# Kernel optimization log

Measured on AMD Instinct MI355X. Metric: run time of the kernel, lower is better.

Reference implementation:

```python
import jax, jax.numpy as jnp
import numpy as np

SOS = 1  # parsed_vocab.index('<SOS>')
D = 1024
V_IN = 8000
V_OUT = 8000


def gru_cell(x, h, W_ih, W_hh, b_ih, b_hh):
    # PyTorch GRU cell: gates ordered [r, z, n]
    gi = x @ W_ih.T + b_ih          # [B, 3D]
    gh = h @ W_hh.T + b_hh          # [B, 3D]
    i_r, i_z, i_n = jnp.split(gi, 3, axis=-1)
    h_r, h_z, h_n = jnp.split(gh, 3, axis=-1)
    r = jax.nn.sigmoid(i_r + h_r)
    z = jax.nn.sigmoid(i_z + h_z)
    n = jnp.tanh(i_n + r * h_n)
    return (1.0 - z) * n + z * h


def setup_inputs() -> dict:
    key = jax.random.key(0)
    ks = jax.random.split(key, 16)
    s = 1.0 / np.sqrt(D)
    f = lambda k, shape: jax.random.uniform(k, shape, jnp.float32, -s, s)
    return {
        "src": jax.random.randint(ks[0], (256, 128), 0, V_IN),
        "tgt": jax.random.randint(ks[1], (128, 128), 0, V_OUT),
        "enc_emb": jax.random.normal(ks[2], (V_IN, D), jnp.float32),
        "enc_W_ih": f(ks[3], (3 * D, D)),
        "enc_W_hh": f(ks[4], (3 * D, D)),
        "enc_b_ih": f(ks[5], (3 * D,)),
        "enc_b_hh": f(ks[6], (3 * D,)),
        "dec_emb": jax.random.normal(ks[7], (V_OUT, D), jnp.float32),
        "dec_W_ih": f(ks[8], (3 * D, D)),
        "dec_W_hh": f(ks[9], (3 * D, D)),
        "dec_b_ih": f(ks[10], (3 * D,)),
        "dec_b_hh": f(ks[11], (3 * D,)),
        "out_W": f(ks[12], (V_OUT, D)),
        "out_b": f(ks[13], (V_OUT,)),
    }


def reference(src, tgt, enc_emb, enc_W_ih, enc_W_hh, enc_b_ih, enc_b_hh,
              dec_emb, dec_W_ih, dec_W_hh, dec_b_ih, dec_b_hh, out_W, out_b):
    B = src.shape[1]
    # ---- Encoder: GRU over src, keep final hidden ----
    xs = enc_emb[src]  # [S_src, B, D]
    h0 = jnp.zeros((B, D), xs.dtype)

    def enc_step(h, x):
        return gru_cell(x, h, enc_W_ih, enc_W_hh, enc_b_ih, enc_b_hh), None

    h_enc, _ = jax.lax.scan(enc_step, h0, xs)

    # ---- Decoder: greedy argmax feedback (eval path, tf_ratio=0) ----
    tok0 = jnp.full((B,), SOS, dtype=src.dtype)

    def dec_step(carry, _):
        h, tok = carry
        x = dec_emb[tok]                                  # [B, D]
        h_new = gru_cell(x, h, dec_W_ih, dec_W_hh, dec_b_ih, dec_b_hh)
        logits = h_new @ out_W.T + out_b                  # [B, V_OUT]
        next_tok = jnp.argmax(logits, axis=-1).astype(tok.dtype)
        return (h_new, next_tok), logits

    target_length = tgt.shape[0]
    _, logits = jax.lax.scan(dec_step, (h_enc, tok0), None, length=target_length)
    return logits  # [S_tgt, B, V_OUT]
```

## Files before the change

### kernel.cpp

```cpp
#include <hip/hip_runtime.h>
#include <math.h>

#define DD    1024
#define BB    128
#define G3    3072
#define VOUT  8000
#define S_SRC 256
#define S_TGT 128
#define SOS   1
#define KS    4
#define KSL   2

__global__ __launch_bounds__(256) void k_init(float* __restrict__ h, int* __restrict__ tok) {
    int idx = blockIdx.x * 256 + threadIdx.x;
    if (idx < BB * DD) h[idx] = 0.0f;
    if (idx < BB) tok[idx] = SOS;
}

__device__ __forceinline__ void gemm_core(
    const float* __restrict__ A0, const float* __restrict__ A1,
    const float* __restrict__ A2, const float* __restrict__ A3,
    const float* __restrict__ Brow, int kbeg, int ntiles,
    float (&acc)[8][2])
{
    __shared__ float As[32][132];
    __shared__ float Bs[32][36];
    const int tid = threadIdx.x;
    const int kq  = (tid & 7) * 4;
    const int r0  = tid >> 3;
    const int tx  = tid & 15, ty = tid >> 4;
    const float* Arow[4] = {A0, A1, A2, A3};

    for (int t = 0; t < ntiles; ++t) {
        const int k0 = kbeg + t * 32;
        #pragma unroll
        for (int p = 0; p < 4; ++p) {
            float4 v = *reinterpret_cast<const float4*>(Arow[p] + k0 + kq);
            int m = r0 + p * 32;
            As[kq+0][m] = v.x; As[kq+1][m] = v.y; As[kq+2][m] = v.z; As[kq+3][m] = v.w;
        }
        {
            float4 v = *reinterpret_cast<const float4*>(Brow + k0 + kq);
            Bs[kq+0][r0] = v.x; Bs[kq+1][r0] = v.y; Bs[kq+2][r0] = v.z; Bs[kq+3][r0] = v.w;
        }
        __syncthreads();
        #pragma unroll
        for (int k = 0; k < 32; ++k) {
            float a[8];
            #pragma unroll
            for (int i = 0; i < 8; ++i) a[i] = As[k][ty*8 + i];
            float b0 = Bs[k][tx*2 + 0], b1 = Bs[k][tx*2 + 1];
            #pragma unroll
            for (int i = 0; i < 8; ++i) {
                acc[i][0] = fmaf(a[i], b0, acc[i][0]);
                acc[i][1] = fmaf(a[i], b1, acc[i][1]);
            }
        }
        __syncthreads();
    }
}

__global__ __launch_bounds__(256) void k_gi_chunk(
    const float* __restrict__ emb, const int* __restrict__ src_c,
    const float* __restrict__ Wih, const float* __restrict__ bih,
    float* __restrict__ gi_buf)
{
    const int n0    = blockIdx.x * 32;
    const int mbase = blockIdx.y * 128;
    const int tid = threadIdx.x;
    const int r0  = tid >> 3;
    const int tx  = tid & 15, ty = tid >> 4;

    const float* A[4];
    #pragma unroll
    for (int p = 0; p < 4; ++p)
        A[p] = emb + (size_t)src_c[mbase + r0 + p * 32] * DD;
    const float* Brow = Wih + (size_t)(n0 + r0) * DD;

    float acc[8][2] = {};
    gemm_core(A[0], A[1], A[2], A[3], Brow, 0, DD / 32, acc);

    #pragma unroll
    for (int i = 0; i < 8; ++i) {
        size_t m = (size_t)(mbase + ty*8 + i);
        #pragma unroll
        for (int j = 0; j < 2; ++j) {
            int n = n0 + tx*2 + j;
            gi_buf[m * G3 + n] = acc[i][j] + bih[n];
        }
    }
}

__global__ __launch_bounds__(256) void k_gates_ks(
    const float* __restrict__ emb, const int* __restrict__ tok,
    const float* __restrict__ h,
    const float* __restrict__ Wih, const float* __restrict__ Whh,
    float* __restrict__ gi_base, float* __restrict__ gh_base,
    int side_base)
{
    const int side = side_base + blockIdx.y;
    const int kh   = blockIdx.z;
    const int kseg = DD / KS;
    const float* __restrict__ W = side ? Whh : Wih;
    float* __restrict__ C = (side ? gh_base : gi_base) + (size_t)kh * (BB * G3);

    const int n0  = blockIdx.x * 32;
    const int tid = threadIdx.x;
    const int r0  = tid >> 3;
    const int tx  = tid & 15, ty = tid >> 4;

    const float* A[4];
    #pragma unroll
    for (int p = 0; p < 4; ++p) {
        int m = r0 + p * 32;
        A[p] = side ? (h + (size_t)m * DD)
                    : (emb + (size_t)tok[m] * DD);
    }
    const float* Brow = W + (size_t)(n0 + r0) * DD;

    float acc[8][2] = {};
    gemm_core(A[0], A[1], A[2], A[3], Brow, kh * kseg, kseg / 32, acc);

    #pragma unroll
    for (int i = 0; i < 8; ++i) {
        size_t m = (size_t)(ty*8 + i);
        C[m * G3 + n0 + tx*2 + 0] = acc[i][0];
        C[m * G3 + n0 + tx*2 + 1] = acc[i][1];
    }
}

__global__ __launch_bounds__(256) void k_logits_ks(
    const float* __restrict__ h, const float* __restrict__ W,
    float* __restrict__ p_base)
{
    const int kh   = blockIdx.y;
    const int kseg = DD / KSL;
    float* __restrict__ C = p_base + (size_t)kh * (BB * VOUT);

    const int n0  = blockIdx.x * 32;
    const int tid = threadIdx.x;
    const int r0  = tid >> 3;
    const int tx  = tid & 15, ty = tid >> 4;

    const float* A[4];
    #pragma unroll
    for (int p = 0; p < 4; ++p) A[p] = h + (size_t)(r0 + p * 32) * DD;
    const float* Brow = W + (size_t)(n0 + r0) * DD;

    float acc[8][2] = {};
    gemm_core(A[0], A[1], A[2], A[3], Brow, kh * kseg, kseg / 32, acc);

    #pragma unroll
    for (int i = 0; i < 8; ++i) {
        size_t m = (size_t)(ty*8 + i);
        C[m * VOUT + n0 + tx*2 + 0] = acc[i][0];
        C[m * VOUT + n0 + tx*2 + 1] = acc[i][1];
    }
}

__global__ __launch_bounds__(256) void k_update(
    const float* __restrict__ gi_base, int ns_i, const float* __restrict__ bih,
    const float* __restrict__ gh_base, int ns_h, const float* __restrict__ bhh,
    float* __restrict__ h)
{
    int idx = blockIdx.x * 256 + threadIdx.x;
    int b = idx >> 10, d = idx & 1023;
    size_t o = (size_t)b * G3 + d;

    float ir = 0.f, iz = 0.f, in_ = 0.f;
    for (int p = 0; p < ns_i; ++p) {
        const float* g = gi_base + (size_t)p * (BB * G3);
        ir += g[o]; iz += g[o + DD]; in_ += g[o + 2*DD];
    }
    if (bih) { ir += bih[d]; iz += bih[DD + d]; in_ += bih[2*DD + d]; }

    float hr = 0.f, hz = 0.f, hn = 0.f;
    for (int p = 0; p < ns_h; ++p) {
        const float* g = gh_base + (size_t)p * (BB * G3);
        hr += g[o]; hz += g[o + DD]; hn += g[o + 2*DD];
    }
    hr += bhh[d]; hz += bhh[DD + d]; hn += bhh[2*DD + d];

    float r = 1.0f / (1.0f + expf(-(ir + hr)));
    float z = 1.0f / (1.0f + expf(-(iz + hz)));
    float n = tanhf(in_ + r * hn);
    float hv = h[idx];
    h[idx] = (1.0f - z) * n + z * hv;
}

__global__ __launch_bounds__(256) void k_argmax_out(
    const float* __restrict__ p0, const float* __restrict__ p1,
    const float* __restrict__ bias,
    float* __restrict__ outC, int* __restrict__ tok)
{
    const int b = blockIdx.x;
    const size_t ro = (size_t)b * VOUT;
    const int tid = threadIdx.x;

    float bv = -INFINITY; int bi = 0x7fffffff;
    for (int v = tid * 4; v < VOUT; v += 1024) {
        float4 a = *reinterpret_cast<const float4*>(p0 + ro + v);
        float4 c = *reinterpret_cast<const float4*>(p1 + ro + v);
        float4 bb = *reinterpret_cast<const float4*>(bias + v);
        float4 r;
        r.x = a.x + c.x + bb.x;
        r.y = a.y + c.y + bb.y;
        r.z = a.z + c.z + bb.z;
        r.w = a.w + c.w + bb.w;
        *reinterpret_cast<float4*>(outC + ro + v) = r;
        if (r.x > bv) { bv = r.x; bi = v + 0; }
        if (r.y > bv) { bv = r.y; bi = v + 1; }
        if (r.z > bv) { bv = r.z; bi = v + 2; }
        if (r.w > bv) { bv = r.w; bi = v + 3; }
    }
    __shared__ float sv[256];
    __shared__ int   si[256];
    sv[tid] = bv; si[tid] = bi;
    __syncthreads();
    for (int s = 128; s > 0; s >>= 1) {
        if (tid < s) {
            if (sv[tid+s] > sv[tid] || (sv[tid+s] == sv[tid] && si[tid+s] < si[tid])) {
                sv[tid] = sv[tid+s]; si[tid] = si[tid+s];
            }
        }
        __syncthreads();
    }
    if (tid == 0) tok[b] = si[0];
}

extern "C" void kernel_launch(void* const* d_in, const int* in_sizes, int n_in,
                              void* d_out, int out_size, void* d_ws, size_t ws_size,
                              hipStream_t stream) {
    const int*   src     = (const int*)  d_in[0];
    const float* enc_emb = (const float*)d_in[2];
    const float* eWih    = (const float*)d_in[3];
    const float* eWhh    = (const float*)d_in[4];
    const float* ebih    = (const float*)d_in[5];
    const float* ebhh    = (const float*)d_in[6];
    const float* dec_emb = (const float*)d_in[7];
    const float* dWih    = (const float*)d_in[8];
    const float* dWhh    = (const float*)d_in[9];
    const float* dbih    = (const float*)d_in[10];
    const float* dbhh    = (const float*)d_in[11];
    const float* outW    = (const float*)d_in[12];
    const float* outb    = (const float*)d_in[13];
    float* out = (float*)d_out;

    float* h    = (float*)d_ws;
    float* gi_p = h + BB * DD;
    float* gh_p = gi_p + KS * BB * G3;
    int*  tok   = (int*)(gh_p + KS * BB * G3);
    float* scratch = (float*)(tok + 256);

    size_t fixed_bytes = (size_t)((char*)scratch - (char*)d_ws);
    int CH = 8;
    while (CH > 1) {
        size_t scr = (size_t)CH * BB * G3;
        size_t scr2 = (size_t)KSL * BB * VOUT;
        if (scr < scr2) scr = scr2;
        if (fixed_bytes + scr * sizeof(float) <= ws_size) break;
        CH >>= 1;
    }
    float* gi_buf = scratch;
    float* p0     = scratch;
    float* p1     = scratch + BB * VOUT;

    k_init<<<512, 256, 0, stream>>>(h, tok);

    for (int c = 0; c < S_SRC; c += CH) {
        k_gi_chunk<<<dim3(96, CH), 256, 0, stream>>>(enc_emb, src + c * BB,
                                                     eWih, ebih, gi_buf);
        for (int s = 0; s < CH; ++s) {
            k_gates_ks<<<dim3(96, 1, KS), 256, 0, stream>>>(enc_emb, tok, h,
                                                            eWih, eWhh,
                                                            nullptr, gh_p, 1);
            k_update<<<512, 256, 0, stream>>>(gi_buf + (size_t)s * BB * G3, 1, nullptr,
                                              gh_p, KS, ebhh, h);
        }
    }

    for (int t = 0; t < S_TGT; ++t) {
        k_gates_ks<<<dim3(96, 2, KS), 256, 0, stream>>>(dec_emb, tok, h,
                                                        dWih, dWhh,
                                                        gi_p, gh_p, 0);
        k_update<<<512, 256, 0, stream>>>(gi_p, KS, dbih, gh_p, KS, dbhh, h);
        k_logits_ks<<<dim3(250, KSL), 256, 0, stream>>>(h, outW, p0);
        float* Ct = out + (size_t)t * BB * VOUT;
        k_argmax_out<<<128, 256, 0, stream>>>(p0, p1, outb, Ct, tok);
    }
}
```

Baseline: 21.16 ms.

## Replace per-step kernel launches with persistent encoder/decoder kernels using grid barriers

```diff
diff --git a/kernel.cpp b/kernel.cpp
--- a/kernel.cpp
+++ b/kernel.cpp
@@ -8,23 +8,37 @@
 #define S_SRC 256
 #define S_TGT 128
 #define SOS   1
-#define KS    4
-#define KSL   2
-
-__global__ __launch_bounds__(256) void k_init(float* __restrict__ h, int* __restrict__ tok) {
+#define GRID  768
+#define KS_F  4
+
+__device__ __forceinline__ void gbar(unsigned* bar) {
+    __syncthreads();
+    if (threadIdx.x == 0) {
+        __threadfence();
+        unsigned old = atomicAdd(bar, 1u);
+        unsigned target = (old / GRID + 1u) * GRID;
+        while (__hip_atomic_load(bar, __ATOMIC_RELAXED, __HIP_MEMORY_SCOPE_AGENT) < target)
+            __builtin_amdgcn_s_sleep(1);
+        __threadfence();
+    }
+    __syncthreads();
+}
+
+__global__ __launch_bounds__(256) void k_init(float* __restrict__ h, int* __restrict__ tok,
+                                              unsigned* __restrict__ bar) {
     int idx = blockIdx.x * 256 + threadIdx.x;
     if (idx < BB * DD) h[idx] = 0.0f;
     if (idx < BB) tok[idx] = SOS;
+    if (idx == 0) bar[0] = 0u;
 }
 
 __device__ __forceinline__ void gemm_core(
+    float (* __restrict__ As)[132], float (* __restrict__ Bs)[34],
     const float* __restrict__ A0, const float* __restrict__ A1,
     const float* __restrict__ A2, const float* __restrict__ A3,
     const float* __restrict__ Brow, int kbeg, int ntiles,
     float (&acc)[8][2])
 {
-    __shared__ float As[32][132];
-    __shared__ float Bs[32][36];
     const int tid = threadIdx.x;
     const int kq  = (tid & 7) * 4;
     const int r0  = tid >> 3;
@@ -60,26 +74,231 @@
     }
 }
 
+
+__global__ __launch_bounds__(256, 3) void k_enc_p(
+    const float* __restrict__ emb, const int* __restrict__ src,
+    const float* __restrict__ Wih, const float* __restrict__ bih,
+    const float* __restrict__ Whh, const float* __restrict__ bhh,
+    float* __restrict__ h, float* __restrict__ gh_p,
+    float* __restrict__ gi_buf, int CH, unsigned* bar)
+{
+    __shared__ float As[32][132];
+    __shared__ float Bs[32][34];
+    const int bid = blockIdx.x, tid = threadIdx.x;
+    const int r0 = tid >> 3, tx = tid & 15, ty = tid >> 4;
+
+    for (int s = 0; s < S_SRC; ++s) {
+        if ((s & (CH - 1)) == 0) {
+            const int cs = bid / 96, nt = bid % 96;
+            if (cs < CH) {
+                const int* srow = src + (s + cs) * BB;
+                const float* A0 = emb + (size_t)srow[r0 +  0] * DD;
+                const float* A1 = emb + (size_t)srow[r0 + 32] * DD;
+                const float* A2 = emb + (size_t)srow[r0 + 64] * DD;
+                const float* A3 = emb + (size_t)srow[r0 + 96] * DD;
+                float acc[8][2] = {};
+                gemm_core(As, Bs, A0, A1, A2, A3,
+                          Wih + (size_t)(nt*32 + r0) * DD, 0, DD/32, acc);
+                float* C = gi_buf + (size_t)cs * (BB * G3);
+                #pragma unroll
+                for (int i = 0; i < 8; ++i) {
+                    int m = ty*8 + i;
+                    #pragma unroll
+                    for (int j = 0; j < 2; ++j) {
+                        int n = nt*32 + tx*2 + j;
+                        C[(size_t)m * G3 + n] = acc[i][j] + bih[n];
+                    }
+                }
+            }
+            gbar(bar);
+        }
+        {
+            const int kh = bid / 96, nt = bid % 96;
+            const float* A0 = h + (size_t)(r0 +  0) * DD;
+            const float* A1 = h + (size_t)(r0 + 32) * DD;
+            const float* A2 = h + (size_t)(r0 + 64) * DD;
+            const float* A3 = h + (size_t)(r0 + 96) * DD;
+            float acc[8][2] = {};
+            gemm_core(As, Bs, A0, A1, A2, A3,
+                      Whh + (size_t)(nt*32 + r0) * DD, kh * 128, 4, acc);
+            float* C = gh_p + (size_t)kh * (BB * G3);
+            #pragma unroll
+            for (int i = 0; i < 8; ++i) {
+                int m = ty*8 + i;
+                C[(size_t)m * G3 + nt*32 + tx*2 + 0] = acc[i][0];
+                C[(size_t)m * G3 + nt*32 + tx*2 + 1] = acc[i][1];
+            }
+        }
+        gbar(bar);
+        {
+            int idx = bid * 256 + tid;
+            if (idx < BB * DD) {
+                int b = idx >> 10, d = idx & 1023;
+                size_t o = (size_t)b * G3 + d;
+                const float* gib = gi_buf + (size_t)(s & (CH-1)) * (BB * G3);
+                float ir = gib[o], iz = gib[o + DD], in_ = gib[o + 2*DD];
+                float hr = bhh[d], hz = bhh[DD + d], hn = bhh[2*DD + d];
+                #pragma unroll
+                for (int p = 0; p < 8; ++p) {
+                    const float* g = gh_p + (size_t)p * (BB * G3);
+                    hr += g[o]; hz += g[o + DD]; hn += g[o + 2*DD];
+                }
+                float r = 1.0f / (1.0f + expf(-(ir + hr)));
+                float z = 1.0f / (1.0f + expf(-(iz + hz)));
+                float n = tanhf(in_ + r * hn);
+                h[idx] = (1.0f - z) * n + z * h[idx];
+            }
+        }
+        gbar(bar);
+    }
+}
+
+__global__ __launch_bounds__(256, 3) void k_dec_p(
+    const float* __restrict__ emb,
+    const float* __restrict__ Wih, const float* __restrict__ bih,
+    const float* __restrict__ Whh, const float* __restrict__ bhh,
+    const float* __restrict__ outW, const float* __restrict__ outb,
+    float* __restrict__ h, float* __restrict__ g_p,
+    float* __restrict__ lg_p, int* __restrict__ tok,
+    float* __restrict__ out, int KSL, unsigned* bar)
+{
+    __shared__ float As[32][132];
+    __shared__ float Bs[32][34];
+    float* sv = &As[0][0];
+    int*   si = (int*)&As[8][0];
+    const int bid = blockIdx.x, tid = threadIdx.x;
+    const int r0 = tid >> 3, tx = tid & 15, ty = tid >> 4;
+
+    for (int t = 0; t < S_TGT; ++t) {
+        {
+            const int side = bid / 384;
+            const int rem  = bid - side * 384;
+            const int kh   = rem / 96, nt = rem % 96;
+            const float *A0, *A1, *A2, *A3;
+            if (side) {
+                A0 = h + (size_t)(r0 +  0) * DD;
+                A1 = h + (size_t)(r0 + 32) * DD;
+                A2 = h + (size_t)(r0 + 64) * DD;
+                A3 = h + (size_t)(r0 + 96) * DD;
+            } else {
+                A0 = emb + (size_t)tok[r0 +  0] * DD;
+                A1 = emb + (size_t)tok[r0 + 32] * DD;
+                A2 = emb + (size_t)tok[r0 + 64] * DD;
+                A3 = emb + (size_t)tok[r0 + 96] * DD;
+            }
+            const float* W = side ? Whh : Wih;
+            float acc[8][2] = {};
+            gemm_core(As, Bs, A0, A1, A2, A3,
+                      W + (size_t)(nt*32 + r0) * DD, kh * 256, 8, acc);
+            float* C = g_p + (size_t)(side*4 + kh) * (BB * G3);
+            #pragma unroll
+            for (int i = 0; i < 8; ++i) {
+                int m = ty*8 + i;
+                C[(size_t)m * G3 + nt*32 + tx*2 + 0] = acc[i][0];
+                C[(size_t)m * G3 + nt*32 + tx*2 + 1] = acc[i][1];
+            }
+        }
+        gbar(bar);
+        {
+            int idx = bid * 256 + tid;
+            if (idx < BB * DD) {
+                int b = idx >> 10, d = idx & 1023;
+                size_t o = (size_t)b * G3 + d;
+                float ir = bih[d], iz = bih[DD + d], in_ = bih[2*DD + d];
+                #pragma unroll
+                for (int p = 0; p < 4; ++p) {
+                    const float* g = g_p + (size_t)p * (BB * G3);
+                    ir += g[o]; iz += g[o + DD]; in_ += g[o + 2*DD];
+                }
+                float hr = bhh[d], hz = bhh[DD + d], hn = bhh[2*DD + d];
+                #pragma unroll
+                for (int p = 4; p < 8; ++p) {
+                    const float* g = g_p + (size_t)p * (BB * G3);
+                    hr += g[o]; hz += g[o + DD]; hn += g[o + 2*DD];
+                }
+                float r = 1.0f / (1.0f + expf(-(ir + hr)));
+                float z = 1.0f / (1.0f + expf(-(iz + hz)));
+                float n = tanhf(in_ + r * hn);
+                h[idx] = (1.0f - z) * n + z * h[idx];
+            }
+        }
+        gbar(bar);
+        {
+            const int kh = bid / 250, nt = bid % 250;
+            if (kh < KSL) {
+                const int t0 = (32 * kh) / KSL, t1 = (32 * (kh + 1)) / KSL;
+                const float* A0 = h + (size_t)(r0 +  0) * DD;
+                const float* A1 = h + (size_t)(r0 + 32) * DD;
+                const float* A2 = h + (size_t)(r0 + 64) * DD;
+                const float* A3 = h + (size_t)(r0 + 96) * DD;
+                float acc[8][2] = {};
+                gemm_core(As, Bs, A0, A1, A2, A3,
+                          outW + (size_t)(nt*32 + r0) * DD, t0 * 32, t1 - t0, acc);
+                float* C = lg_p + (size_t)kh * (BB * VOUT);
+                #pragma unroll
+                for (int i = 0; i < 8; ++i) {
+                    int m = ty*8 + i;
+                    C[(size_t)m * VOUT + nt*32 + tx*2 + 0] = acc[i][0];
+                    C[(size_t)m * VOUT + nt*32 + tx*2 + 1] = acc[i][1];
+                }
+            }
+        }
+        gbar(bar);
+        if (bid < BB) {
+            const int b = bid;
+            const size_t ro = (size_t)b * VOUT;
+            float* Ct = out + (size_t)t * (BB * VOUT) + ro;
+            float bv = -INFINITY; int bi = 0x7fffffff;
+            for (int v = tid * 4; v < VOUT; v += 1024) {
+                float4 rr = *reinterpret_cast<const float4*>(outb + v);
+                for (int kh = 0; kh < KSL; ++kh) {
+                    float4 p = *reinterpret_cast<const float4*>(
+                        lg_p + (size_t)kh * (BB * VOUT) + ro + v);
+                    rr.x += p.x; rr.y += p.y; rr.z += p.z; rr.w += p.w;
+                }
+                *reinterpret_cast<float4*>(Ct + v) = rr;
+                if (rr.x > bv) { bv = rr.x; bi = v + 0; }
+                if (rr.y > bv) { bv = rr.y; bi = v + 1; }
+                if (rr.z > bv) { bv = rr.z; bi = v + 2; }
+                if (rr.w > bv) { bv = rr.w; bi = v + 3; }
+            }
+            sv[tid] = bv; si[tid] = bi;
+            __syncthreads();
+            for (int st = 128; st > 0; st >>= 1) {
+                if (tid < st) {
+                    if (sv[tid+st] > sv[tid] ||
+                        (sv[tid+st] == sv[tid] && si[tid+st] < si[tid])) {
+                        sv[tid] = sv[tid+st]; si[tid] = si[tid+st];
+                    }
+                }
+                __syncthreads();
+            }
+            if (tid == 0) tok[b] = si[0];
+        }
+        gbar(bar);
+    }
+}
+
+
 __global__ __launch_bounds__(256) void k_gi_chunk(
     const float* __restrict__ emb, const int* __restrict__ src_c,
     const float* __restrict__ Wih, const float* __restrict__ bih,
     float* __restrict__ gi_buf)
 {
+    __shared__ float As[32][132];
+    __shared__ float Bs[32][34];
     const int n0    = blockIdx.x * 32;
     const int mbase = blockIdx.y * 128;
     const int tid = threadIdx.x;
-    const int r0  = tid >> 3;
-    const int tx  = tid & 15, ty = tid >> 4;
+    const int r0  = tid >> 3, tx = tid & 15, ty = tid >> 4;
 
     const float* A[4];
     #pragma unroll
     for (int p = 0; p < 4; ++p)
         A[p] = emb + (size_t)src_c[mbase + r0 + p * 32] * DD;
-    const float* Brow = Wih + (size_t)(n0 + r0) * DD;
-
     float acc[8][2] = {};
-    gemm_core(A[0], A[1], A[2], A[3], Brow, 0, DD / 32, acc);
-
+    gemm_core(As, Bs, A[0], A[1], A[2], A[3],
+              Wih + (size_t)(n0 + r0) * DD, 0, DD/32, acc);
     #pragma unroll
     for (int i = 0; i < 8; ++i) {
         size_t m = (size_t)(mbase + ty*8 + i);
@@ -98,29 +317,27 @@
     float* __restrict__ gi_base, float* __restrict__ gh_base,
     int side_base)
 {
+    __shared__ float As[32][132];
+    __shared__ float Bs[32][34];
     const int side = side_base + blockIdx.y;
     const int kh   = blockIdx.z;
-    const int kseg = DD / KS;
+    const int kseg = DD / KS_F;
     const float* __restrict__ W = side ? Whh : Wih;
     float* __restrict__ C = (side ? gh_base : gi_base) + (size_t)kh * (BB * G3);
 
     const int n0  = blockIdx.x * 32;
     const int tid = threadIdx.x;
-    const int r0  = tid >> 3;
-    const int tx  = tid & 15, ty = tid >> 4;
+    const int r0  = tid >> 3, tx = tid & 15, ty = tid >> 4;
 
     const float* A[4];
     #pragma unroll
     for (int p = 0; p < 4; ++p) {
         int m = r0 + p * 32;
-        A[p] = side ? (h + (size_t)m * DD)
-                    : (emb + (size_t)tok[m] * DD);
-    }
-    const float* Brow = W + (size_t)(n0 + r0) * DD;
-
+        A[p] = side ? (h + (size_t)m * DD) : (emb + (size_t)tok[m] * DD);
+    }
     float acc[8][2] = {};
-    gemm_core(A[0], A[1], A[2], A[3], Brow, kh * kseg, kseg / 32, acc);
-
+    gemm_core(As, Bs, A[0], A[1], A[2], A[3],
+              W + (size_t)(n0 + r0) * DD, kh * kseg, kseg / 32, acc);
     #pragma unroll
     for (int i = 0; i < 8; ++i) {
         size_t m = (size_t)(ty*8 + i);
@@ -133,23 +350,22 @@
     const float* __restrict__ h, const float* __restrict__ W,
     float* __restrict__ p_base)
 {
+    __shared__ float As[32][132];
+    __shared__ float Bs[32][34];
     const int kh   = blockIdx.y;
-    const int kseg = DD / KSL;
+    const int kseg = DD / 2;
     float* __restrict__ C = p_base + (size_t)kh * (BB * VOUT);
 
     const int n0  = blockIdx.x * 32;
     const int tid = threadIdx.x;
-    const int r0  = tid >> 3;
-    const int tx  = tid & 15, ty = tid >> 4;
+    const int r0  = tid >> 3, tx = tid & 15, ty = tid >> 4;
 
     const float* A[4];
     #pragma unroll
     for (int p = 0; p < 4; ++p) A[p] = h + (size_t)(r0 + p * 32) * DD;
-    const float* Brow = W + (size_t)(n0 + r0) * DD;
-
     float acc[8][2] = {};
-    gemm_core(A[0], A[1], A[2], A[3], Brow, kh * kseg, kseg / 32, acc);
-
+    gemm_core(As, Bs, A[0], A[1], A[2], A[3],
+              W + (size_t)(n0 + r0) * DD, kh * kseg, kseg / 32, acc);
     #pragma unroll
     for (int i = 0; i < 8; ++i) {
         size_t m = (size_t)(ty*8 + i);
@@ -158,7 +374,7 @@
     }
 }
 
-__global__ __launch_bounds__(256) void k_update(
+__global__ __launch_bounds__(256) void k_update_f(
     const float* __restrict__ gi_base, int ns_i, const float* __restrict__ bih,
     const float* __restrict__ gh_base, int ns_h, const float* __restrict__ bhh,
     float* __restrict__ h)
@@ -247,45 +463,66 @@
     float* out = (float*)d_out;
 
     float* h    = (float*)d_ws;
-    float* gi_p = h + BB * DD;
-    float* gh_p = gi_p + KS * BB * G3;
-    int*  tok   = (int*)(gh_p + KS * BB * G3);
+    float* g_p  = h + BB * DD;
+    int*  tok   = (int*)(g_p + 8 * BB * G3);
+    unsigned* bar = (unsigned*)(tok + 128);
     float* scratch = (float*)(tok + 256);
 
-    size_t fixed_bytes = (size_t)((char*)scratch - (char*)d_ws);
+    size_t fixed = (size_t)((char*)scratch - (char*)d_ws);
+    size_t avail = (ws_size > fixed) ? ws_size - fixed : 0;
+    int KSLv = (avail >= (size_t)3 * BB * VOUT * 4) ? 3 : 2;
     int CH = 8;
-    while (CH > 1) {
-        size_t scr = (size_t)CH * BB * G3;
-        size_t scr2 = (size_t)KSL * BB * VOUT;
-        if (scr < scr2) scr = scr2;
-        if (fixed_bytes + scr * sizeof(float) <= ws_size) break;
-        CH >>= 1;
-    }
+    while (CH > 1 && (size_t)CH * BB * G3 * 4 > avail) CH >>= 1;
+
     float* gi_buf = scratch;
-    float* p0     = scratch;
-    float* p1     = scratch + BB * VOUT;
-
-    k_init<<<512, 256, 0, stream>>>(h, tok);
-
-    for (int c = 0; c < S_SRC; c += CH) {
-        k_gi_chunk<<<dim3(96, CH), 256, 0, stream>>>(enc_emb, src + c * BB,
-                                                     eWih, ebih, gi_buf);
-        for (int s = 0; s < CH; ++s) {
-            k_gates_ks<<<dim3(96, 1, KS), 256, 0, stream>>>(enc_emb, tok, h,
-                                                            eWih, eWhh,
-                                                            nullptr, gh_p, 1);
-            k_update<<<512, 256, 0, stream>>>(gi_buf + (size_t)s * BB * G3, 1, nullptr,
-                                              gh_p, KS, ebhh, h);
-        }
-    }
-
-    for (int t = 0; t < S_TGT; ++t) {
-        k_gates_ks<<<dim3(96, 2, KS), 256, 0, stream>>>(dec_emb, tok, h,
-                                                        dWih, dWhh,
-                                                        gi_p, gh_p, 0);
-        k_update<<<512, 256, 0, stream>>>(gi_p, KS, dbih, gh_p, KS, dbhh, h);
-        k_logits_ks<<<dim3(250, KSL), 256, 0, stream>>>(h, outW, p0);
-        float* Ct = out + (size_t)t * BB * VOUT;
-        k_argmax_out<<<128, 256, 0, stream>>>(p0, p1, outb, Ct, tok);
-    }
-}
+    float* lg_p   = scratch;
+
+    static int persist_ok = -1;
+    if (persist_ok < 0) {
+        int nb_e = 0, nb_d = 0, ncu = 0, dev = 0;
+        hipError_t e0 = hipGetDevice(&dev);
+        hipError_t e1 = hipOccupancyMaxActiveBlocksPerMultiprocessor(
+            &nb_e, (const void*)k_enc_p, 256, 0);
+        hipError_t e2 = hipOccupancyMaxActiveBlocksPerMultiprocessor(
+            &nb_d, (const void*)k_dec_p, 256, 0);
+        hipError_t e3 = hipDeviceGetAttribute(
+            &ncu, hipDeviceAttributeMultiprocessorCount, dev);
+        persist_ok = (e0 == hipSuccess && e1 == hipSuccess && e2 == hipSuccess &&
+                      e3 == hipSuccess && nb_e >= 3 && nb_d >= 3 &&
+                      (long)ncu * 3 >= GRID) ? 1 : 0;
+    }
+
+    k_init<<<512, 256, 0, stream>>>(h, tok, bar);
+
+    if (persist_ok == 1) {
+        k_enc_p<<<GRID, 256, 0, stream>>>(enc_emb, src, eWih, ebih, eWhh, ebhh,
+                                          h, g_p, gi_buf, CH, bar);
+        k_dec_p<<<GRID, 256, 0, stream>>>(dec_emb, dWih, dbih, dWhh, dbhh,
+                                          outW, outb, h, g_p, lg_p, tok,
+                                          out, KSLv, bar);
+    } else {
+        float* gi_p = g_p;
+        float* gh_p = g_p + 4 * BB * G3;
+        float* p0   = scratch;
+        float* p1   = scratch + BB * VOUT;
+
+        for (int c = 0; c < S_SRC; c += CH) {
+            k_gi_chunk<<<dim3(96, CH), 256, 0, stream>>>(enc_emb, src + c * BB,
+                                                         eWih, ebih, gi_buf);
+            for (int s = 0; s < CH; ++s) {
+                k_gates_ks<<<dim3(96, 1, KS_F), 256, 0, stream>>>(
+                    enc_emb, tok, h, eWih, eWhh, nullptr, gh_p, 1);
+                k_update_f<<<512, 256, 0, stream>>>(
+                    gi_buf + (size_t)s * BB * G3, 1, nullptr, gh_p, KS_F, ebhh, h);
+            }
+        }
+        for (int t = 0; t < S_TGT; ++t) {
+            k_gates_ks<<<dim3(96, 2, KS_F), 256, 0, stream>>>(
+                dec_emb, tok, h, dWih, dWhh, gi_p, gh_p, 0);
+            k_update_f<<<512, 256, 0, stream>>>(gi_p, KS_F, dbih, gh_p, KS_F, dbhh, h);
+            k_logits_ks<<<dim3(250, 2), 256, 0, stream>>>(h, outW, p0);
+            float* Ct = out + (size_t)t * BB * VOUT;
+            k_argmax_out<<<128, 256, 0, stream>>>(p0, p1, outb, Ct, tok);
+        }
+    }
+}
```

New measurement: 24.48 ms. +15.7%, slower.
